# Optimization experiments

Hardware: AMD Instinct MI355X
Metric: run time of the kernel (lower is better)

## Reference

```python
import jax, jax.numpy as jnp
import numpy as np

B, NSP, H, W = 8, 1024, 256, 256   # frames, superpixels/frame, label-map size
N = B * NSP                        # total superpixel nodes
MIX = 0.5                          # mixing_coeff
SIGMA = 0.05


def _interp_axis(x, out, axis):
    # 1-D bilinear interpolation along `axis`, align_corners=True
    n = x.shape[axis]
    pos = jnp.linspace(0.0, n - 1.0, out).astype(x.dtype)
    i0 = jnp.floor(pos).astype(jnp.int32)
    i1 = jnp.minimum(i0 + 1, n - 1)
    wt = pos - i0.astype(x.dtype)
    shp = [1] * x.ndim
    shp[axis] = out
    wt = wt.reshape(shp)
    return jnp.take(x, i0, axis=axis) * (1 - wt) + jnp.take(x, i1, axis=axis) * wt


def _upsample_ac(x, oh, ow):
    # nn.UpsamplingBilinear2d (align_corners=True)
    if x.shape[2] == oh and x.shape[3] == ow:
        return x
    return _interp_axis(_interp_axis(x, oh, 2), ow, 3)


def _sp_pool(feats, seg):
    # upsample [B,C,h,w] to label resolution, then average features per superpixel -> [N, C]
    C = feats.shape[1]
    up = _upsample_ac(feats, H, W)
    vals = up.transpose(0, 2, 3, 1).reshape(-1, C)          # [B*H*W, C]
    sums = jax.ops.segment_sum(vals, seg, num_segments=N)
    cnt = jax.ops.segment_sum(jnp.ones((seg.shape[0],), vals.dtype), seg, num_segments=N)
    return sums / jnp.maximum(cnt, 1.0)[:, None]


def _gcn(x, Wm, b, src, dst, ew):
    # GCNConv(normalize=False): out_i = sum_{j->i} ew * (x_j @ W) + b
    h = x @ Wm
    agg = jax.ops.segment_sum(h[src] * ew[:, None], dst, num_segments=x.shape[0])
    return agg + b


def _coord_map():
    # channel 0 varies along dim2 (w), channel 1 varies along dim3 (h), both in [0,1]
    c0 = jnp.broadcast_to((jnp.arange(H, dtype=jnp.float32) / (H - 1))[:, None], (H, W))
    c1 = jnp.broadcast_to((jnp.arange(W, dtype=jnp.float32) / (W - 1))[None, :], (H, W))
    return jnp.broadcast_to(jnp.stack([c0, c1], 0)[None], (B, 2, H, W))


def setup_inputs() -> dict:
    key = jax.random.key(0)
    ks = jax.random.split(key, 12)
    labels = jax.random.randint(ks[0], (B, 1, H, W), 0, NSP, dtype=jnp.int32)
    skip0 = jax.random.normal(ks[1], (B, 512, 32, 32), jnp.float32)
    skip1 = jax.random.normal(ks[2], (B, 256, 64, 64), jnp.float32)
    skip2 = jax.random.normal(ks[3], (B, 256, 128, 128), jnp.float32)
    E = 131072
    edges_nn = jax.random.randint(ks[4], (2, E), 0, N, dtype=jnp.int32)
    negs = jax.random.randint(ks[5], (E,), 0, N, dtype=jnp.int32)
    W0 = jax.random.normal(ks[6], (512, 256), jnp.float32) / np.float32(np.sqrt(512))
    W1 = jax.random.normal(ks[7], (256, 256), jnp.float32) / np.float32(np.sqrt(256))
    W2 = jax.random.normal(ks[8], (256, 256), jnp.float32) / np.float32(np.sqrt(256))
    lin_w = jax.random.normal(ks[9], (256, 1), jnp.float32) / np.float32(np.sqrt(256))
    z = jnp.zeros((256,), jnp.float32)
    return {"labels": labels, "skip0": skip0, "skip1": skip1, "skip2": skip2,
            "edges_nn": edges_nn, "negs": negs,
            "W0": W0, "b0": z, "W1": W1, "b1": z, "W2": W2, "b2": z, "lin_w": lin_w}


def reference(labels, skip0, skip1, skip2, edges_nn, negs, W0, b0, W1, b1, W2, b2, lin_w):
    # per-pixel global superpixel id (offset per frame)
    seg = (labels.reshape(B, -1) + NSP * jnp.arange(B, dtype=labels.dtype)[:, None]).reshape(-1)
    src, dst = edges_nn[0], edges_nn[1]

    # pooled normalized coordinates per superpixel -> gaussian edge weights
    pc = _sp_pool(_coord_map(), seg)                        # [N, 2]
    dr = pc[src] - pc[dst]
    dist = jnp.linalg.norm(dr, axis=1)
    edge_attr = jnp.exp(-dist ** 2 / SIGMA)

    x = _sp_pool(skip0, seg)                                # [N, 512]
    layers = [(W0, b0, None), (W1, b1, skip1), (W2, b2, skip2)]
    for i, (Wm, b, sk) in enumerate(layers):
        if i > 0:
            x = (1 - MIX) * x + MIX * _sp_pool(sk, seg)
        x = jax.nn.relu(_gcn(x, Wm, b, src, dst, edge_attr))

    s = x @ lin_w                                           # [N, 1]
    dap = jax.nn.sigmoid(s[src] - s[dst])
    dan = jax.nn.sigmoid(s[src] - s[negs])
    return dan, dap, edge_attr
```

## Files before the change

### kernel.cpp

```cpp
#include <hip/hip_runtime.h>
#include <hip/hip_fp16.h>
#include <cstdint>
#include <cstddef>

#define BB 8
#define NSPX 1024
#define NNODE 8192
#define EE 131072
#define NPIX 524288
#define CH 256

typedef unsigned int uint;
typedef unsigned long long u64;

__device__ __forceinline__ uint packh2(float a, float b) {
  __half2 h = __float22half2_rn(make_float2(a, b));
  return *reinterpret_cast<uint*>(&h);
}
__device__ __forceinline__ __half2 uh2(uint u) { return *reinterpret_cast<__half2*>(&u); }
__device__ __forceinline__ uint h2u(__half2 h) { return *reinterpret_cast<uint*>(&h); }

__global__ __launch_bounds__(256) void zero_kernel(int4* p, int n4) {
  int i = blockIdx.x * 256 + threadIdx.x;
  int stride = gridDim.x * 256;
  int4 z = make_int4(0, 0, 0, 0);
  for (; i < n4; i += stride) p[i] = z;
}

__device__ __forceinline__ void dev_transpose_h(const float* __restrict__ src, __half* __restrict__ dst,
                                                int C, int P, int b, int p0, int c0, int t,
                                                uint (*tile)[33]) {
  int l16 = t & 15, r16 = t >> 4;
#pragma unroll
  for (int pass = 0; pass < 4; ++pass) {
    int c = r16 + pass * 16;
    float4 v = *(const float4*)&src[((size_t)b * C + c0 + c) * P + p0 + l16 * 4];
    tile[c][l16 * 2]     = packh2(v.x, v.y);
    tile[c][l16 * 2 + 1] = packh2(v.z, v.w);
  }
  __syncthreads();
  int l8 = t & 7, r32 = t >> 3;
#pragma unroll
  for (int pass = 0; pass < 2; ++pass) {
    int p = r32 + pass * 32;
    int ph = p >> 1;
    int odd = p & 1;
    uint r[4];
#pragma unroll
    for (int q = 0; q < 4; ++q) {
      uint ua = tile[l8 * 8 + 2 * q][ph];
      uint ub = tile[l8 * 8 + 2 * q + 1][ph];
      r[q] = odd ? ((ua >> 16) | (ub & 0xFFFF0000u))
                 : ((ua & 0xFFFFu) | (ub << 16));
    }
    *(uint4*)&dst[((size_t)b * P + p0 + p) * C + c0 + l8 * 8] = make_uint4(r[0], r[1], r[2], r[3]);
  }
}

__global__ __launch_bounds__(256) void t2_kernel(const float* __restrict__ src, __half* __restrict__ dst) {
  __shared__ uint tile[64][33];
  int idx = blockIdx.x;
  int p0 = (idx & 255) * 64;
  int c0 = ((idx >> 8) & 3) * 64;
  int b = idx >> 10;
  dev_transpose_h(src, dst, 256, 16384, b, p0, c0, threadIdx.x, tile);
}

__device__ __forceinline__ void dev_gemm_kmaj(const float* __restrict__ A, const float* __restrict__ W,
                                              __half* __restrict__ out, int idx, int t,
                                              float (*As)[36]) {
  int b = idx >> 6;
  int m0 = (idx & 31) * 32;
  int n0 = ((idx >> 5) & 1) * 128;
  int ct = t & 31;
  int rm = t >> 5;
  int l8 = t & 7, kr = t >> 3;
  const float* Ab = A + (size_t)b * 512 * 1024;
  float4 acc[4];
#pragma unroll
  for (int i = 0; i < 4; ++i) acc[i] = make_float4(0.f, 0.f, 0.f, 0.f);
  for (int k0 = 0; k0 < 512; k0 += 64) {
#pragma unroll
    for (int pass = 0; pass < 2; ++pass) {
      int k = kr + pass * 32;
      float4 v = *(const float4*)&Ab[(size_t)(k0 + k) * 1024 + m0 + l8 * 4];
      *(float4*)&As[k][l8 * 4] = v;
    }
    __syncthreads();
#pragma unroll 8
    for (int k = 0; k < 64; ++k) {
      float4 a = *(const float4*)&As[k][rm * 4];
      float4 wv = *(const float4*)&W[(size_t)(k0 + k) * 256 + n0 + ct * 4];
      acc[0].x += a.x * wv.x; acc[0].y += a.x * wv.y; acc[0].z += a.x * wv.z; acc[0].w += a.x * wv.w;
      acc[1].x += a.y * wv.x; acc[1].y += a.y * wv.y; acc[1].z += a.y * wv.z; acc[1].w += a.y * wv.w;
      acc[2].x += a.z * wv.x; acc[2].y += a.z * wv.y; acc[2].z += a.z * wv.z; acc[2].w += a.z * wv.w;
      acc[3].x += a.w * wv.x; acc[3].y += a.w * wv.y; acc[3].z += a.w * wv.z; acc[3].w += a.w * wv.w;
    }
    __syncthreads();
  }
#pragma unroll
  for (int i = 0; i < 4; ++i) {
    int m = m0 + rm * 4 + i;
    uint2 pk = make_uint2(packh2(acc[i].x, acc[i].y), packh2(acc[i].z, acc[i].w));
    *(uint2*)&out[((size_t)b * 1024 + m) * 256 + n0 + ct * 4] = pk;
  }
}

__global__ __launch_bounds__(256) void fusedA2_kernel(const int* __restrict__ labels,
                                                      const int* __restrict__ edst,
                                                      int* __restrict__ segb,
                                                      u64* __restrict__ packed,
                                                      int* __restrict__ cnt_e,
                                                      const float* __restrict__ skip0,
                                                      const float* __restrict__ W0,
                                                      __half* __restrict__ F0b,
                                                      const float* __restrict__ skip1,
                                                      __half* __restrict__ F1t) {
  __shared__ __align__(16) char smem[9216];
  int blk = blockIdx.x;
  int t = threadIdx.x;
  int s = blk % 10;
  int q = blk / 10;
  if (s < 4) {
    int idx = q * 4 + s;
    int p0 = (idx & 63) * 64;
    int c0 = ((idx >> 6) & 3) * 64;
    int b = idx >> 8;
    dev_transpose_h(skip1, F1t, 256, 4096, b, p0, c0, t, (uint(*)[33])smem);
  } else if (s < 9) {
    int idx = q * 5 + (s - 4);
    if (idx < 2048) {
      int p = idx * 256 + t;
      int b = p >> 16;
      int h = (p >> 8) & 255;
      int w = p & 255;
      int seg = labels[p] + (b << 10);
      segb[p] = seg;
      u64 enc = (1ULL << 48) | ((u64)h << 24) | (u64)w;
      atomicAdd(&packed[seg], enc);
    } else {
      int e = (idx - 2048) * 256 + t;
      atomicAdd(&cnt_e[edst[e]], 1);
    }
  } else {
    dev_gemm_kmaj(skip0, W0, F0b, q, t, (float(*)[36])smem);
  }
}

__global__ __launch_bounds__(1024) void fusedB_kernel(const u64* __restrict__ packed,
                                                      const int* __restrict__ cnt_e,
                                                      int* __restrict__ poff, int* __restrict__ eoff,
                                                      float* __restrict__ rcnt,
                                                      float* __restrict__ pch, float* __restrict__ pcw) {
  int blk = blockIdx.x;
  int t = threadIdx.x;
  if (blk < 2) {
    __shared__ int ps[1024];
    int which = blk;
    int* coff = which ? eoff : poff;
    int base = t * 8;
    int v[8];
    int sum = 0;
#pragma unroll
    for (int i = 0; i < 8; ++i) {
      int x = which ? cnt_e[base + i] : (int)(packed[base + i] >> 48);
      v[i] = sum;
      sum += x;
    }
    ps[t] = sum;
    __syncthreads();
    for (int off = 1; off < 1024; off <<= 1) {
      int x = (t >= off) ? ps[t - off] : 0;
      __syncthreads();
      ps[t] += x;
      __syncthreads();
    }
    int prev = (t == 0) ? 0 : ps[t - 1];
#pragma unroll
    for (int i = 0; i < 8; ++i) coff[base + i] = prev + v[i];
    if (t == 1023) coff[8192] = ps[1023];
  } else {
    int n = (blk - 2) * 1024 + t;
    u64 v = packed[n];
    int c = (int)(v >> 48);
    int sh = (int)((v >> 24) & 0xFFFFFF);
    int sw = (int)(v & 0xFFFFFF);
    float r = 1.0f / (float)(c > 1 ? c : 1);
    rcnt[n] = r;
    pch[n] = (float)sh * r * (1.0f / 255.0f);
    pcw[n] = (float)sw * r * (1.0f / 255.0f);
  }
}

__global__ __launch_bounds__(256) void scatter2_kernel(const int* __restrict__ segb,
                                                       const int* __restrict__ poff,
                                                       int* __restrict__ pcur,
                                                       int* __restrict__ psorted,
                                                       const int* __restrict__ esrc,
                                                       const int* __restrict__ edst,
                                                       const float* __restrict__ pch,
                                                       const float* __restrict__ pcw,
                                                       const int* __restrict__ eoff,
                                                       int* __restrict__ ecur,
                                                       uint2* __restrict__ evw,
                                                       float* __restrict__ outp) {
  int blk = blockIdx.x;
  int t = threadIdx.x;
  if (blk < 2048) {
    int p = blk * 256 + t;
    int s = segb[p];
    int pos = poff[s] + atomicAdd(&pcur[s], 1);
    psorted[pos] = p;
  } else {
    int e = (blk - 2048) * 256 + t;
    int s1 = esrc[e], d1 = edst[e];
    float dh = pch[s1] - pch[d1];
    float dw = pcw[s1] - pcw[d1];
    float ea = expf(-(dh * dh + dw * dw) * 20.0f);
    outp[2 * EE + e] = ea;
    int pos = eoff[d1] + atomicAdd(&ecur[d1], 1);
    evw[pos] = make_uint2((uint)s1, __float_as_uint(ea));
  }
}

__device__ __forceinline__ void tap16(const __half* __restrict__ tp, float wt, __half2* acc) {
  uint4 qa = *(const uint4*)tp;
  uint4 qb = *(const uint4*)(tp + 8);
  __half2 W = __float2half2_rn(wt);
  acc[0] = __hfma2(W, uh2(qa.x), acc[0]);
  acc[1] = __hfma2(W, uh2(qa.y), acc[1]);
  acc[2] = __hfma2(W, uh2(qa.z), acc[2]);
  acc[3] = __hfma2(W, uh2(qa.w), acc[3]);
  acc[4] = __hfma2(W, uh2(qb.x), acc[4]);
  acc[5] = __hfma2(W, uh2(qb.y), acc[5]);
  acc[6] = __hfma2(W, uh2(qb.z), acc[6]);
  acc[7] = __hfma2(W, uh2(qb.w), acc[7]);
}

template <int HS>
__device__ __forceinline__ void taps16(const __half* __restrict__ fb, int h, int w, __half2* acc) {
  const float fh = (float)(HS - 1) / 255.0f;
  float ph = h * fh, pw = w * fh;
  int i0 = (int)ph, j0 = (int)pw;
  float th = ph - (float)i0, tw = pw - (float)j0;
  int i1 = min(i0 + 1, HS - 1), jj1 = min(j0 + 1, HS - 1);
  float w11 = th * tw, w10 = th - w11, w01 = tw - w11, w00 = 1.f - th - tw + w11;
  tap16(fb + (i0 * HS + j0) * 256, w00, acc);
  tap16(fb + (i0 * HS + jj1) * 256, w01, acc);
  tap16(fb + (i1 * HS + j0) * 256, w10, acc);
  tap16(fb + (i1 * HS + jj1) * 256, w11, acc);
}

__global__ __launch_bounds__(256) void fusedC_kernel(const __half* __restrict__ F0,
                                                     const __half* __restrict__ F1,
                                                     const __half* __restrict__ F2,
                                                     const int* __restrict__ poff,
                                                     const int* __restrict__ psorted,
                                                     const float* __restrict__ rc,
                                                     __half* __restrict__ p0out,
                                                     float* __restrict__ p1out,
                                                     float* __restrict__ p2out) {
  __shared__ __align__(16) char smem[18432];
  int blk = blockIdx.x;
  int t = threadIdx.x;
  if (blk >= 8192 && blk < 16384) {
    int x = blk - 8192;
    int n = ((x & 7) << 10) | (x >> 3);
    int b = n >> 10;
    int l = t & 15;
    int s = t >> 4;
    const __half* f0 = F0 + (size_t)b * 1024 * 256 + l * 16;
    const __half* f1 = F1 + (size_t)b * 4096 * 256 + l * 16;
    int j1 = poff[n + 1];
    __half2 z = __float2half2_rn(0.f);
    __half2 a0[8], a1[8];
#pragma unroll
    for (int i = 0; i < 8; ++i) { a0[i] = z; a1[i] = z; }
    for (int j = poff[n] + s; j < j1; j += 16) {
      int p = psorted[j];
      int h = (p >> 8) & 255, w = p & 255;
      taps16<32>(f0, h, w, a0);
      taps16<64>(f1, h, w, a1);
    }
    uint (*red)[256][9] = (uint(*)[256][9])smem;
#pragma unroll
    for (int k = 0; k < 8; ++k) { red[0][t][k] = h2u(a0[k]); red[1][t][k] = h2u(a1[k]); }
    __syncthreads();
    if (t < 128) {
      int l2 = t >> 3, k = t & 7;
      float r = rc[n];
      float2 s0 = make_float2(0.f, 0.f), s1 = s0;
#pragma unroll
      for (int ss = 0; ss < 16; ++ss) {
        float2 v0 = __half22float2(uh2(red[0][ss * 16 + l2][k]));
        float2 v1 = __half22float2(uh2(red[1][ss * 16 + l2][k]));
        s0.x += v0.x; s0.y += v0.y;
        s1.x += v1.x; s1.y += v1.y;
      }
      int c = l2 * 16 + k * 2;
      *(uint*)&p0out[(size_t)n * 256 + c] = packh2(s0.x * r, s0.y * r);
      *(float2*)&p1out[(size_t)n * 256 + c] = make_float2(s1.x * r, s1.y * r);
    }
  } else {
    int x, c0;
    if (blk < 8192) { x = blk; c0 = 0; }
    else            { x = blk - 16384; c0 = 128; }
    int n = ((x & 7) << 10) | (x >> 3);
    int b = n >> 10;
    int l = t & 7;
    int s = t >> 3;
    const __half* fb = F2 + (size_t)b * 16384 * 256 + c0 + l * 16;
    int j1 = poff[n + 1];
    __half2 z = __float2half2_rn(0.f);
    __half2 acc[8];
#pragma unroll
    for (int i = 0; i < 8; ++i) acc[i] = z;
    for (int j = poff[n] + s; j < j1; j += 32) {
      int p = psorted[j];
      int h = (p >> 8) & 255, w = p & 255;
      taps16<128>(fb, h, w, acc);
    }
    uint (*red)[9] = (uint(*)[9])smem;
#pragma unroll
    for (int k = 0; k < 8; ++k) red[t][k] = h2u(acc[k]);
    __syncthreads();
    if (t < 64) {
      int l2 = t >> 3, k = t & 7;
      float r = rc[n];
      float2 sm = make_float2(0.f, 0.f);
#pragma unroll
      for (int ss = 0; ss < 32; ++ss) {
        float2 v = __half22float2(uh2(red[ss * 8 + l2][k]));
        sm.x += v.x; sm.y += v.y;
      }
      int c = c0 + l2 * 16 + k * 2;
      *(float2*)&p2out[(size_t)n * 256 + c] = make_float2(sm.x * r, sm.y * r);
    }
  }
}

__global__ __launch_bounds__(256) void gemm_mix_n256(const float* __restrict__ X, const float* __restrict__ Pl,
                                                     const float* __restrict__ W, __half* __restrict__ out) {
  const int t = threadIdx.x;
  const int r0 = blockIdx.x * 16;
  const int cw = (t & 63) * 4;
  const int rg = (t >> 6) * 4;
  __shared__ float Xl[16][68];
  float4 acc[4];
#pragma unroll
  for (int i = 0; i < 4; ++i) acc[i] = make_float4(0.f, 0.f, 0.f, 0.f);
  for (int k0 = 0; k0 < 256; k0 += 64) {
#pragma unroll
    for (int l = 0; l < 4; ++l) {
      int idx = t + 256 * l;
      int r = idx >> 6, k = idx & 63;
      size_t a = (size_t)(r0 + r) * 256 + k0 + k;
      Xl[r][k] = 0.5f * (X[a] + Pl[a]);
    }
    __syncthreads();
#pragma unroll
    for (int k4 = 0; k4 < 64; k4 += 4) {
      float4 a[4];
#pragma unroll
      for (int i = 0; i < 4; ++i) a[i] = *(const float4*)&Xl[rg + i][k4];
#pragma unroll
      for (int kk = 0; kk < 4; ++kk) {
        float4 w = *(const float4*)&W[(size_t)(k0 + k4 + kk) * 256 + cw];
#pragma unroll
        for (int i = 0; i < 4; ++i) {
          float av = ((const float*)&a[i])[kk];
          acc[i].x += av * w.x;
          acc[i].y += av * w.y;
          acc[i].z += av * w.z;
          acc[i].w += av * w.w;
        }
      }
    }
    __syncthreads();
  }
#pragma unroll
  for (int i = 0; i < 4; ++i) {
    uint2 pk = make_uint2(packh2(acc[i].x, acc[i].y), packh2(acc[i].z, acc[i].w));
    *(uint2*)&out[(size_t)(r0 + rg + i) * 256 + cw] = pk;
  }
}

__global__ __launch_bounds__(256) void agg_kernel(const __half* __restrict__ h, const float* __restrict__ bias,
                                                  const int* __restrict__ eoff,
                                                  const uint2* __restrict__ evw,
                                                  float* __restrict__ xout) {
  int n = blockIdx.x * 2 + (threadIdx.x >> 7);
  int c2 = threadIdx.x & 127;
  int e0 = eoff[n], e1 = eoff[n + 1];
  float a0 = 0.f, a1 = 0.f;
  for (int j = e0; j < e1; ++j) {
    uint2 ev = evw[j];
    float wv = __uint_as_float(ev.y);
    uint hv = *(const uint*)&h[((size_t)ev.x << 8) + c2 * 2];
    float2 f = __half22float2(uh2(hv));
    a0 += wv * f.x;
    a1 += wv * f.y;
  }
  float v0 = a0 + bias[2 * c2];
  float v1 = a1 + bias[2 * c2 + 1];
  float2 st = make_float2(v0 > 0.f ? v0 : 0.f, v1 > 0.f ? v1 : 0.f);
  *(float2*)&xout[((size_t)n << 8) + 2 * c2] = st;
}

__global__ __launch_bounds__(256) void score_kernel(const float* __restrict__ x, const float* __restrict__ lw,
                                                    float* __restrict__ s) {
  int t = threadIdx.x;
  int n = blockIdx.x * 4 + (t >> 6);
  int lane = t & 63;
  const float* row = x + ((size_t)n << 8);
  float v = row[lane] * lw[lane] + row[lane + 64] * lw[lane + 64] +
            row[lane + 128] * lw[lane + 128] + row[lane + 192] * lw[lane + 192];
#pragma unroll
  for (int off = 32; off > 0; off >>= 1) v += __shfl_down(v, off, 64);
  if (lane == 0) s[n] = v;
}

__global__ __launch_bounds__(256) void out_kernel(const float* __restrict__ s, const int* __restrict__ src,
                                                  const int* __restrict__ dst, const int* __restrict__ negs,
                                                  float* __restrict__ outp) {
  int e = blockIdx.x * 256 + threadIdx.x;
  if (e >= EE) return;
  float ss = s[src[e]];
  float a = ss - s[negs[e]];
  float b = ss - s[dst[e]];
  outp[e] = 1.0f / (1.0f + expf(-a));
  outp[EE + e] = 1.0f / (1.0f + expf(-b));
}

extern "C" void kernel_launch(void* const* d_in, const int* in_sizes, int n_in,
                              void* d_out, int out_size, void* d_ws, size_t ws_size,
                              hipStream_t stream) {
  const int*   labels = (const int*)d_in[0];
  const float* skip0  = (const float*)d_in[1];
  const float* skip1  = (const float*)d_in[2];
  const float* skip2  = (const float*)d_in[3];
  const int*   edges  = (const int*)d_in[4];
  const int*   negs   = (const int*)d_in[5];
  const float* W0     = (const float*)d_in[6];
  const float* b0     = (const float*)d_in[7];
  const float* W1     = (const float*)d_in[8];
  const float* b1     = (const float*)d_in[9];
  const float* W2     = (const float*)d_in[10];
  const float* b2     = (const float*)d_in[11];
  const float* lw     = (const float*)d_in[12];
  const int* esrc = edges;
  const int* edst = edges + EE;
  float* outp = (float*)d_out;

  size_t o = 0;
  char* base = (char*)d_ws;
  auto alloc = [&](size_t bytes) -> void* {
    void* p = base + o;
    o += (bytes + 255) & ~(size_t)255;
    return p;
  };
  u64* packed  = (u64*)alloc(NNODE * 8);
  int* cnt_e   = (int*)alloc(NNODE * 4);
  int* ecur    = (int*)alloc(NNODE * 4);
  int* pcur    = (int*)alloc(NNODE * 4);
  size_t zbytes = o;
  float*  rcnt    = (float*)alloc(NNODE * 4);
  float*  pch     = (float*)alloc(NNODE * 4);
  float*  pcw     = (float*)alloc(NNODE * 4);
  int*    poff    = (int*)alloc((NNODE + 1) * 4);
  int*    eoff    = (int*)alloc((NNODE + 1) * 4);
  uint2*  evw     = (uint2*)alloc((size_t)EE * 8);
  int*    psorted = (int*)alloc(NPIX * 4);
  int*    segb    = (int*)alloc(NPIX * 4);
  float*  bufA    = (float*)alloc((size_t)NNODE * CH * 4);
  float*  bufB    = (float*)alloc((size_t)NNODE * CH * 4);
  float*  p1buf   = (float*)alloc((size_t)NNODE * CH * 4);
  float*  p2buf   = (float*)alloc((size_t)NNODE * CH * 4);
  __half* h0b     = (__half*)alloc((size_t)NNODE * CH * 2);
  __half* h1b     = (__half*)alloc((size_t)NNODE * CH * 2);
  __half* F0b     = (__half*)alloc((size_t)BB * 1024 * CH * 2);
  __half* F1t     = (__half*)alloc((size_t)BB * 4096 * CH * 2);
  __half* F2t     = (__half*)alloc((size_t)BB * 16384 * CH * 2);
  float*  sbuf    = (float*)alloc(NNODE * 4);
  (void)ws_size; (void)n_in; (void)in_sizes; (void)out_size;

  zero_kernel<<<64, 256, 0, stream>>>((int4*)d_ws, (int)(zbytes / 16));
  fusedA2_kernel<<<5120, 256, 0, stream>>>(labels, edst, segb, packed, cnt_e,
                                           skip0, W0, F0b, skip1, F1t);
  t2_kernel<<<8192, 256, 0, stream>>>(skip2, F2t);
  fusedB_kernel<<<10, 1024, 0, stream>>>(packed, cnt_e, poff, eoff, rcnt, pch, pcw);
  scatter2_kernel<<<2048 + 512, 256, 0, stream>>>(segb, poff, pcur, psorted,
                                                  esrc, edst, pch, pcw, eoff, ecur, evw, outp);
  fusedC_kernel<<<24576, 256, 0, stream>>>(F0b, F1t, F2t, poff, psorted, rcnt,
                                           h0b, p1buf, p2buf);
  agg_kernel<<<NNODE / 2, 256, 0, stream>>>(h0b, b0, eoff, evw, bufB);
  gemm_mix_n256<<<NNODE / 16, 256, 0, stream>>>(bufB, p1buf, W1, h1b);
  agg_kernel<<<NNODE / 2, 256, 0, stream>>>(h1b, b1, eoff, evw, bufA);
  gemm_mix_n256<<<NNODE / 16, 256, 0, stream>>>(bufA, p2buf, W2, h1b);
  agg_kernel<<<NNODE / 2, 256, 0, stream>>>(h1b, b2, eoff, evw, bufB);
  score_kernel<<<NNODE / 4, 256, 0, stream>>>(bufB, lw, sbuf);
  out_kernel<<<EE / 256, 256, 0, stream>>>(sbuf, esrc, edst, negs, outp);
}
```

Before: 731.0 us.

## Fuse GCN tail into one cooperative kernel and regroup transpose launches

The seven small tail launches (three aggregations, two mix GEMMs, score, output) become a single cooperative persistent kernel of 1024 blocks that uses grid-wide syncs between stages. If the cooperative launch fails, it falls back to the original separate launches. The skip2 and skip1 transposes move out of the first fused kernel and the standalone transpose kernel into the pixel-scatter and edge-weight kernel. The aim is to cut launch gaps and overlap the memory-bound transposes with the atomic scatter work, at the cost of grid-sync overhead and fewer active blocks per stage.

```diff
diff --git a/kernel.cpp b/kernel.cpp
--- a/kernel.cpp
+++ b/kernel.cpp
@@ -1,7 +1,10 @@
 #include <hip/hip_runtime.h>
 #include <hip/hip_fp16.h>
+#include <hip/hip_cooperative_groups.h>
 #include <cstdint>
 #include <cstddef>
+
+namespace cg = cooperative_groups;
 
 #define BB 8
 #define NSPX 1024
@@ -55,15 +58,6 @@
     }
     *(uint4*)&dst[((size_t)b * P + p0 + p) * C + c0 + l8 * 8] = make_uint4(r[0], r[1], r[2], r[3]);
   }
-}
-
-__global__ __launch_bounds__(256) void t2_kernel(const float* __restrict__ src, __half* __restrict__ dst) {
-  __shared__ uint tile[64][33];
-  int idx = blockIdx.x;
-  int p0 = (idx & 255) * 64;
-  int c0 = ((idx >> 8) & 3) * 64;
-  int b = idx >> 10;
-  dev_transpose_h(src, dst, 256, 16384, b, p0, c0, threadIdx.x, tile);
 }
 
 __device__ __forceinline__ void dev_gemm_kmaj(const float* __restrict__ A, const float* __restrict__ W,
@@ -106,31 +100,20 @@
   }
 }
 
-__global__ __launch_bounds__(256) void fusedA2_kernel(const int* __restrict__ labels,
+__global__ __launch_bounds__(256) void fusedA3_kernel(const int* __restrict__ labels,
                                                       const int* __restrict__ edst,
                                                       int* __restrict__ segb,
                                                       u64* __restrict__ packed,
                                                       int* __restrict__ cnt_e,
                                                       const float* __restrict__ skip0,
                                                       const float* __restrict__ W0,
-                                                      __half* __restrict__ F0b,
-                                                      const float* __restrict__ skip1,
-                                                      __half* __restrict__ F1t) {
-  __shared__ __align__(16) char smem[9216];
+                                                      __half* __restrict__ F0b) {
+  __shared__ __align__(16) float As[64][36];
   int blk = blockIdx.x;
   int t = threadIdx.x;
-  int s = blk % 10;
-  int q = blk / 10;
-  if (s < 4) {
-    int idx = q * 4 + s;
-    int p0 = (idx & 63) * 64;
-    int c0 = ((idx >> 6) & 3) * 64;
-    int b = idx >> 8;
-    dev_transpose_h(skip1, F1t, 256, 4096, b, p0, c0, t, (uint(*)[33])smem);
-  } else if (s < 9) {
-    int idx = q * 5 + (s - 4);
-    if (idx < 2048) {
-      int p = idx * 256 + t;
+  if (blk < 2560) {
+    if (blk < 2048) {
+      int p = blk * 256 + t;
       int b = p >> 16;
       int h = (p >> 8) & 255;
       int w = p & 255;
@@ -139,11 +122,11 @@
       u64 enc = (1ULL << 48) | ((u64)h << 24) | (u64)w;
       atomicAdd(&packed[seg], enc);
     } else {
-      int e = (idx - 2048) * 256 + t;
+      int e = (blk - 2048) * 256 + t;
       atomicAdd(&cnt_e[edst[e]], 1);
     }
   } else {
-    dev_gemm_kmaj(skip0, W0, F0b, q, t, (float(*)[36])smem);
+    dev_gemm_kmaj(skip0, W0, F0b, blk - 2560, t, As);
   }
 }
 
@@ -192,34 +175,57 @@
   }
 }
 
-__global__ __launch_bounds__(256) void scatter2_kernel(const int* __restrict__ segb,
-                                                       const int* __restrict__ poff,
-                                                       int* __restrict__ pcur,
-                                                       int* __restrict__ psorted,
-                                                       const int* __restrict__ esrc,
-                                                       const int* __restrict__ edst,
-                                                       const float* __restrict__ pch,
-                                                       const float* __restrict__ pcw,
-                                                       const int* __restrict__ eoff,
-                                                       int* __restrict__ ecur,
-                                                       uint2* __restrict__ evw,
-                                                       float* __restrict__ outp) {
+__global__ __launch_bounds__(256) void fusedT_kernel(const float* __restrict__ skip1,
+                                                     __half* __restrict__ F1t,
+                                                     const float* __restrict__ skip2,
+                                                     __half* __restrict__ F2t,
+                                                     const int* __restrict__ segb,
+                                                     const int* __restrict__ poff,
+                                                     int* __restrict__ pcur,
+                                                     int* __restrict__ psorted,
+                                                     const int* __restrict__ esrc,
+                                                     const int* __restrict__ edst,
+                                                     const float* __restrict__ pch,
+                                                     const float* __restrict__ pcw,
+                                                     const int* __restrict__ eoff,
+                                                     int* __restrict__ ecur,
+                                                     uint2* __restrict__ evw,
+                                                     float* __restrict__ outp) {
+  __shared__ uint tile[64][33];
   int blk = blockIdx.x;
   int t = threadIdx.x;
-  if (blk < 2048) {
-    int p = blk * 256 + t;
-    int s = segb[p];
-    int pos = poff[s] + atomicAdd(&pcur[s], 1);
-    psorted[pos] = p;
+  int s = blk % 5;
+  int q = blk / 5;
+  if (s < 4) {
+    int idx = q * 4 + s;
+    if (idx < 8192) {
+      int p0 = (idx & 255) * 64;
+      int c0 = ((idx >> 8) & 3) * 64;
+      int b = idx >> 10;
+      dev_transpose_h(skip2, F2t, 256, 16384, b, p0, c0, t, tile);
+    } else {
+      int i2 = idx - 8192;
+      int p0 = (i2 & 63) * 64;
+      int c0 = ((i2 >> 6) & 3) * 64;
+      int b = i2 >> 8;
+      dev_transpose_h(skip1, F1t, 256, 4096, b, p0, c0, t, tile);
+    }
   } else {
-    int e = (blk - 2048) * 256 + t;
-    int s1 = esrc[e], d1 = edst[e];
-    float dh = pch[s1] - pch[d1];
-    float dw = pcw[s1] - pcw[d1];
-    float ea = expf(-(dh * dh + dw * dw) * 20.0f);
-    outp[2 * EE + e] = ea;
-    int pos = eoff[d1] + atomicAdd(&ecur[d1], 1);
-    evw[pos] = make_uint2((uint)s1, __float_as_uint(ea));
+    if (q < 2048) {
+      int p = q * 256 + t;
+      int sg = segb[p];
+      int pos = poff[sg] + atomicAdd(&pcur[sg], 1);
+      psorted[pos] = p;
+    } else {
+      int e = (q - 2048) * 256 + t;
+      int s1 = esrc[e], d1 = edst[e];
+      float dh = pch[s1] - pch[d1];
+      float dw = pcw[s1] - pcw[d1];
+      float ea = expf(-(dh * dh + dw * dw) * 20.0f);
+      outp[2 * EE + e] = ea;
+      int pos = eoff[d1] + atomicAdd(&ecur[d1], 1);
+      evw[pos] = make_uint2((uint)s1, __float_as_uint(ea));
+    }
   }
 }
 
@@ -339,58 +345,11 @@
   }
 }
 
-__global__ __launch_bounds__(256) void gemm_mix_n256(const float* __restrict__ X, const float* __restrict__ Pl,
-                                                     const float* __restrict__ W, __half* __restrict__ out) {
-  const int t = threadIdx.x;
-  const int r0 = blockIdx.x * 16;
-  const int cw = (t & 63) * 4;
-  const int rg = (t >> 6) * 4;
-  __shared__ float Xl[16][68];
-  float4 acc[4];
-#pragma unroll
-  for (int i = 0; i < 4; ++i) acc[i] = make_float4(0.f, 0.f, 0.f, 0.f);
-  for (int k0 = 0; k0 < 256; k0 += 64) {
-#pragma unroll
-    for (int l = 0; l < 4; ++l) {
-      int idx = t + 256 * l;
-      int r = idx >> 6, k = idx & 63;
-      size_t a = (size_t)(r0 + r) * 256 + k0 + k;
-      Xl[r][k] = 0.5f * (X[a] + Pl[a]);
-    }
-    __syncthreads();
-#pragma unroll
-    for (int k4 = 0; k4 < 64; k4 += 4) {
-      float4 a[4];
-#pragma unroll
-      for (int i = 0; i < 4; ++i) a[i] = *(const float4*)&Xl[rg + i][k4];
-#pragma unroll
-      for (int kk = 0; kk < 4; ++kk) {
-        float4 w = *(const float4*)&W[(size_t)(k0 + k4 + kk) * 256 + cw];
-#pragma unroll
-        for (int i = 0; i < 4; ++i) {
-          float av = ((const float*)&a[i])[kk];
-          acc[i].x += av * w.x;
-          acc[i].y += av * w.y;
-          acc[i].z += av * w.z;
-          acc[i].w += av * w.w;
-        }
-      }
-    }
-    __syncthreads();
-  }
-#pragma unroll
-  for (int i = 0; i < 4; ++i) {
-    uint2 pk = make_uint2(packh2(acc[i].x, acc[i].y), packh2(acc[i].z, acc[i].w));
-    *(uint2*)&out[(size_t)(r0 + rg + i) * 256 + cw] = pk;
-  }
-}
-
-__global__ __launch_bounds__(256) void agg_kernel(const __half* __restrict__ h, const float* __restrict__ bias,
-                                                  const int* __restrict__ eoff,
-                                                  const uint2* __restrict__ evw,
-                                                  float* __restrict__ xout) {
-  int n = blockIdx.x * 2 + (threadIdx.x >> 7);
-  int c2 = threadIdx.x & 127;
+__device__ __forceinline__ void agg_body(const __half* h, const float* bias,
+                                         const int* eoff, const uint2* evw,
+                                         float* xout, int pr, int t) {
+  int n = pr * 2 + (t >> 7);
+  int c2 = t & 127;
   int e0 = eoff[n], e1 = eoff[n + 1];
   float a0 = 0.f, a1 = 0.f;
   for (int j = e0; j < e1; ++j) {
@@ -403,14 +362,56 @@
   }
   float v0 = a0 + bias[2 * c2];
   float v1 = a1 + bias[2 * c2 + 1];
-  float2 st = make_float2(v0 > 0.f ? v0 : 0.f, v1 > 0.f ? v1 : 0.f);
-  *(float2*)&xout[((size_t)n << 8) + 2 * c2] = st;
-}
-
-__global__ __launch_bounds__(256) void score_kernel(const float* __restrict__ x, const float* __restrict__ lw,
-                                                    float* __restrict__ s) {
-  int t = threadIdx.x;
-  int n = blockIdx.x * 4 + (t >> 6);
+  *(float2*)&xout[((size_t)n << 8) + 2 * c2] =
+      make_float2(v0 > 0.f ? v0 : 0.f, v1 > 0.f ? v1 : 0.f);
+}
+
+__device__ __forceinline__ void gemm_body(const float* X, const float* Pl, const float* W,
+                                          __half* out, int tilei, int t, float (*Xl)[68]) {
+  const int r0 = tilei * 16;
+  const int cw = (t & 63) * 4;
+  const int rg = (t >> 6) * 4;
+  float4 acc[4];
+#pragma unroll
+  for (int i = 0; i < 4; ++i) acc[i] = make_float4(0.f, 0.f, 0.f, 0.f);
+  for (int k0 = 0; k0 < 256; k0 += 64) {
+#pragma unroll
+    for (int l = 0; l < 4; ++l) {
+      int idx = t + 256 * l;
+      int r = idx >> 6, k = idx & 63;
+      size_t a = (size_t)(r0 + r) * 256 + k0 + k;
+      Xl[r][k] = 0.5f * (X[a] + Pl[a]);
+    }
+    __syncthreads();
+#pragma unroll
+    for (int k4 = 0; k4 < 64; k4 += 4) {
+      float4 a[4];
+#pragma unroll
+      for (int i = 0; i < 4; ++i) a[i] = *(const float4*)&Xl[rg + i][k4];
+#pragma unroll
+      for (int kk = 0; kk < 4; ++kk) {
+        float4 w = *(const float4*)&W[(size_t)(k0 + k4 + kk) * 256 + cw];
+#pragma unroll
+        for (int i = 0; i < 4; ++i) {
+          float av = ((const float*)&a[i])[kk];
+          acc[i].x += av * w.x;
+          acc[i].y += av * w.y;
+          acc[i].z += av * w.z;
+          acc[i].w += av * w.w;
+        }
+      }
+    }
+    __syncthreads();
+  }
+#pragma unroll
+  for (int i = 0; i < 4; ++i) {
+    uint2 pk = make_uint2(packh2(acc[i].x, acc[i].y), packh2(acc[i].z, acc[i].w));
+    *(uint2*)&out[(size_t)(r0 + rg + i) * 256 + cw] = pk;
+  }
+}
+
+__device__ __forceinline__ void score_body(const float* x, const float* lw, float* s, int g, int t) {
+  int n = g * 4 + (t >> 6);
   int lane = t & 63;
   const float* row = x + ((size_t)n << 8);
   float v = row[lane] * lw[lane] + row[lane + 64] * lw[lane + 64] +
@@ -418,6 +419,60 @@
 #pragma unroll
   for (int off = 32; off > 0; off >>= 1) v += __shfl_down(v, off, 64);
   if (lane == 0) s[n] = v;
+}
+
+__global__ __launch_bounds__(256, 4) void coop_tail(const __half* h0, const float* b0,
+                                                    const float* b1, const float* b2,
+                                                    const float* W1, const float* W2,
+                                                    const float* lw,
+                                                    const int* eoff, const uint2* evw,
+                                                    const float* p1, const float* p2,
+                                                    float* xA, float* xB, __half* hbuf,
+                                                    float* sbuf,
+                                                    const int* esrc, const int* edst,
+                                                    const int* negs, float* outp) {
+  cg::grid_group grid = cg::this_grid();
+  __shared__ float Xl[16][68];
+  int bid = blockIdx.x;
+  int t = threadIdx.x;
+  for (int pr = bid; pr < 4096; pr += 1024) agg_body(h0, b0, eoff, evw, xB, pr, t);
+  grid.sync();
+  if (bid < 512) gemm_body(xB, p1, W1, hbuf, bid, t, Xl);
+  grid.sync();
+  for (int pr = bid; pr < 4096; pr += 1024) agg_body(hbuf, b1, eoff, evw, xA, pr, t);
+  grid.sync();
+  if (bid < 512) gemm_body(xA, p2, W2, hbuf, bid, t, Xl);
+  grid.sync();
+  for (int pr = bid; pr < 4096; pr += 1024) agg_body(hbuf, b2, eoff, evw, xB, pr, t);
+  grid.sync();
+  for (int g = bid; g < 2048; g += 1024) score_body(xB, lw, sbuf, g, t);
+  grid.sync();
+  for (int g = bid; g < 512; g += 1024) {
+    int e = g * 256 + t;
+    float ss = sbuf[esrc[e]];
+    float a = ss - sbuf[negs[e]];
+    float b = ss - sbuf[edst[e]];
+    outp[e] = 1.0f / (1.0f + expf(-a));
+    outp[EE + e] = 1.0f / (1.0f + expf(-b));
+  }
+}
+
+__global__ __launch_bounds__(256) void agg_kernel(const __half* __restrict__ h, const float* __restrict__ bias,
+                                                  const int* __restrict__ eoff,
+                                                  const uint2* __restrict__ evw,
+                                                  float* __restrict__ xout) {
+  agg_body(h, bias, eoff, evw, xout, blockIdx.x, threadIdx.x);
+}
+
+__global__ __launch_bounds__(256) void gemm_mix_n256(const float* __restrict__ X, const float* __restrict__ Pl,
+                                                     const float* __restrict__ W, __half* __restrict__ out) {
+  __shared__ float Xl[16][68];
+  gemm_body(X, Pl, W, out, blockIdx.x, threadIdx.x, Xl);
+}
+
+__global__ __launch_bounds__(256) void score_kernel(const float* __restrict__ x, const float* __restrict__ lw,
+                                                    float* __restrict__ s) {
+  score_body(x, lw, s, blockIdx.x, threadIdx.x);
 }
 
 __global__ __launch_bounds__(256) void out_kernel(const float* __restrict__ s, const int* __restrict__ src,
@@ -485,19 +540,29 @@
   (void)ws_size; (void)n_in; (void)in_sizes; (void)out_size;
 
   zero_kernel<<<64, 256, 0, stream>>>((int4*)d_ws, (int)(zbytes / 16));
-  fusedA2_kernel<<<5120, 256, 0, stream>>>(labels, edst, segb, packed, cnt_e,
-                                           skip0, W0, F0b, skip1, F1t);
-  t2_kernel<<<8192, 256, 0, stream>>>(skip2, F2t);
+  fusedA3_kernel<<<3072, 256, 0, stream>>>(labels, edst, segb, packed, cnt_e,
+                                           skip0, W0, F0b);
   fusedB_kernel<<<10, 1024, 0, stream>>>(packed, cnt_e, poff, eoff, rcnt, pch, pcw);
-  scatter2_kernel<<<2048 + 512, 256, 0, stream>>>(segb, poff, pcur, psorted,
-                                                  esrc, edst, pch, pcw, eoff, ecur, evw, outp);
+  fusedT_kernel<<<12800, 256, 0, stream>>>(skip1, F1t, skip2, F2t,
+                                           segb, poff, pcur, psorted,
+                                           esrc, edst, pch, pcw, eoff, ecur, evw, outp);
   fusedC_kernel<<<24576, 256, 0, stream>>>(F0b, F1t, F2t, poff, psorted, rcnt,
                                            h0b, p1buf, p2buf);
-  agg_kernel<<<NNODE / 2, 256, 0, stream>>>(h0b, b0, eoff, evw, bufB);
-  gemm_mix_n256<<<NNODE / 16, 256, 0, stream>>>(bufB, p1buf, W1, h1b);
-  agg_kernel<<<NNODE / 2, 256, 0, stream>>>(h1b, b1, eoff, evw, bufA);
-  gemm_mix_n256<<<NNODE / 16, 256, 0, stream>>>(bufA, p2buf, W2, h1b);
-  agg_kernel<<<NNODE / 2, 256, 0, stream>>>(h1b, b2, eoff, evw, bufB);
-  score_kernel<<<NNODE / 4, 256, 0, stream>>>(bufB, lw, sbuf);
-  out_kernel<<<EE / 256, 256, 0, stream>>>(sbuf, esrc, edst, negs, outp);
-}
+  void* cargs[] = {(void*)&h0b, (void*)&b0, (void*)&b1, (void*)&b2,
+                   (void*)&W1, (void*)&W2, (void*)&lw,
+                   (void*)&eoff, (void*)&evw, (void*)&p1buf, (void*)&p2buf,
+                   (void*)&bufA, (void*)&bufB, (void*)&h1b, (void*)&sbuf,
+                   (void*)&esrc, (void*)&edst, (void*)&negs, (void*)&outp};
+  hipError_t cerr = hipLaunchCooperativeKernel((const void*)coop_tail,
+                                               dim3(1024), dim3(256), cargs, 0, stream);
+  if (cerr != hipSuccess) {
+    (void)hipGetLastError();
+    agg_kernel<<<NNODE / 2, 256, 0, stream>>>(h0b, b0, eoff, evw, bufB);
+    gemm_mix_n256<<<NNODE / 16, 256, 0, stream>>>(bufB, p1buf, W1, h1b);
+    agg_kernel<<<NNODE / 2, 256, 0, stream>>>(h1b, b1, eoff, evw, bufA);
+    gemm_mix_n256<<<NNODE / 16, 256, 0, stream>>>(bufA, p2buf, W2, h1b);
+    agg_kernel<<<NNODE / 2, 256, 0, stream>>>(h1b, b2, eoff, evw, bufB);
+    score_kernel<<<NNODE / 4, 256, 0, stream>>>(bufB, lw, sbuf);
+    out_kernel<<<EE / 256, 256, 0, stream>>>(sbuf, esrc, edst, negs, outp);
+  }
+}
```

After: 1.423 ms. +94.6%, slower.

## Regroup launch schedule: fuse transposes and gemm with scatter, fuse final agg with score

Applied to the files above, without the earlier changes.

Splits the counting atomics into their own small kernel and moves the skip1/skip2 transposes and the skip0 gemm into one combined kernel with the pixel/edge scatter, running after the prefix-sum stage. It also fuses the last aggregation with the score dot product so the final node features never go to memory. The aim is fewer launches and better overlap of bandwidth-heavy transposes with the atomic-bound scatter. The trade-off is that the large transposes now wait until the counting and prefix stages finish instead of running alongside them.

```diff
diff --git a/kernel.cpp b/kernel.cpp
--- a/kernel.cpp
+++ b/kernel.cpp
@@ -27,123 +27,25 @@
   for (; i < n4; i += stride) p[i] = z;
 }
 
-__device__ __forceinline__ void dev_transpose_h(const float* __restrict__ src, __half* __restrict__ dst,
-                                                int C, int P, int b, int p0, int c0, int t,
-                                                uint (*tile)[33]) {
-  int l16 = t & 15, r16 = t >> 4;
-#pragma unroll
-  for (int pass = 0; pass < 4; ++pass) {
-    int c = r16 + pass * 16;
-    float4 v = *(const float4*)&src[((size_t)b * C + c0 + c) * P + p0 + l16 * 4];
-    tile[c][l16 * 2]     = packh2(v.x, v.y);
-    tile[c][l16 * 2 + 1] = packh2(v.z, v.w);
-  }
-  __syncthreads();
-  int l8 = t & 7, r32 = t >> 3;
-#pragma unroll
-  for (int pass = 0; pass < 2; ++pass) {
-    int p = r32 + pass * 32;
-    int ph = p >> 1;
-    int odd = p & 1;
-    uint r[4];
-#pragma unroll
-    for (int q = 0; q < 4; ++q) {
-      uint ua = tile[l8 * 8 + 2 * q][ph];
-      uint ub = tile[l8 * 8 + 2 * q + 1][ph];
-      r[q] = odd ? ((ua >> 16) | (ub & 0xFFFF0000u))
-                 : ((ua & 0xFFFFu) | (ub << 16));
-    }
-    *(uint4*)&dst[((size_t)b * P + p0 + p) * C + c0 + l8 * 8] = make_uint4(r[0], r[1], r[2], r[3]);
-  }
-}
-
-__global__ __launch_bounds__(256) void t2_kernel(const float* __restrict__ src, __half* __restrict__ dst) {
-  __shared__ uint tile[64][33];
-  int idx = blockIdx.x;
-  int p0 = (idx & 255) * 64;
-  int c0 = ((idx >> 8) & 3) * 64;
-  int b = idx >> 10;
-  dev_transpose_h(src, dst, 256, 16384, b, p0, c0, threadIdx.x, tile);
-}
-
-__device__ __forceinline__ void dev_gemm_kmaj(const float* __restrict__ A, const float* __restrict__ W,
-                                              __half* __restrict__ out, int idx, int t,
-                                              float (*As)[36]) {
-  int b = idx >> 6;
-  int m0 = (idx & 31) * 32;
-  int n0 = ((idx >> 5) & 1) * 128;
-  int ct = t & 31;
-  int rm = t >> 5;
-  int l8 = t & 7, kr = t >> 3;
-  const float* Ab = A + (size_t)b * 512 * 1024;
-  float4 acc[4];
-#pragma unroll
-  for (int i = 0; i < 4; ++i) acc[i] = make_float4(0.f, 0.f, 0.f, 0.f);
-  for (int k0 = 0; k0 < 512; k0 += 64) {
-#pragma unroll
-    for (int pass = 0; pass < 2; ++pass) {
-      int k = kr + pass * 32;
-      float4 v = *(const float4*)&Ab[(size_t)(k0 + k) * 1024 + m0 + l8 * 4];
-      *(float4*)&As[k][l8 * 4] = v;
-    }
-    __syncthreads();
-#pragma unroll 8
-    for (int k = 0; k < 64; ++k) {
-      float4 a = *(const float4*)&As[k][rm * 4];
-      float4 wv = *(const float4*)&W[(size_t)(k0 + k) * 256 + n0 + ct * 4];
-      acc[0].x += a.x * wv.x; acc[0].y += a.x * wv.y; acc[0].z += a.x * wv.z; acc[0].w += a.x * wv.w;
-      acc[1].x += a.y * wv.x; acc[1].y += a.y * wv.y; acc[1].z += a.y * wv.z; acc[1].w += a.y * wv.w;
-      acc[2].x += a.z * wv.x; acc[2].y += a.z * wv.y; acc[2].z += a.z * wv.z; acc[2].w += a.z * wv.w;
-      acc[3].x += a.w * wv.x; acc[3].y += a.w * wv.y; acc[3].z += a.w * wv.z; acc[3].w += a.w * wv.w;
-    }
-    __syncthreads();
-  }
-#pragma unroll
-  for (int i = 0; i < 4; ++i) {
-    int m = m0 + rm * 4 + i;
-    uint2 pk = make_uint2(packh2(acc[i].x, acc[i].y), packh2(acc[i].z, acc[i].w));
-    *(uint2*)&out[((size_t)b * 1024 + m) * 256 + n0 + ct * 4] = pk;
-  }
-}
-
-__global__ __launch_bounds__(256) void fusedA2_kernel(const int* __restrict__ labels,
-                                                      const int* __restrict__ edst,
-                                                      int* __restrict__ segb,
-                                                      u64* __restrict__ packed,
-                                                      int* __restrict__ cnt_e,
-                                                      const float* __restrict__ skip0,
-                                                      const float* __restrict__ W0,
-                                                      __half* __restrict__ F0b,
-                                                      const float* __restrict__ skip1,
-                                                      __half* __restrict__ F1t) {
-  __shared__ __align__(16) char smem[9216];
+__global__ __launch_bounds__(256) void cnt2_kernel(const int* __restrict__ labels,
+                                                   const int* __restrict__ edst,
+                                                   int* __restrict__ segb,
+                                                   u64* __restrict__ packed,
+                                                   int* __restrict__ cnt_e) {
   int blk = blockIdx.x;
   int t = threadIdx.x;
-  int s = blk % 10;
-  int q = blk / 10;
-  if (s < 4) {
-    int idx = q * 4 + s;
-    int p0 = (idx & 63) * 64;
-    int c0 = ((idx >> 6) & 3) * 64;
-    int b = idx >> 8;
-    dev_transpose_h(skip1, F1t, 256, 4096, b, p0, c0, t, (uint(*)[33])smem);
-  } else if (s < 9) {
-    int idx = q * 5 + (s - 4);
-    if (idx < 2048) {
-      int p = idx * 256 + t;
-      int b = p >> 16;
-      int h = (p >> 8) & 255;
-      int w = p & 255;
-      int seg = labels[p] + (b << 10);
-      segb[p] = seg;
-      u64 enc = (1ULL << 48) | ((u64)h << 24) | (u64)w;
-      atomicAdd(&packed[seg], enc);
-    } else {
-      int e = (idx - 2048) * 256 + t;
-      atomicAdd(&cnt_e[edst[e]], 1);
-    }
+  if (blk < 2048) {
+    int p = blk * 256 + t;
+    int b = p >> 16;
+    int h = (p >> 8) & 255;
+    int w = p & 255;
+    int seg = labels[p] + (b << 10);
+    segb[p] = seg;
+    u64 enc = (1ULL << 48) | ((u64)h << 24) | (u64)w;
+    atomicAdd(&packed[seg], enc);
   } else {
-    dev_gemm_kmaj(skip0, W0, F0b, q, t, (float(*)[36])smem);
+    int e = (blk - 2048) * 256 + t;
+    atomicAdd(&cnt_e[edst[e]], 1);
   }
 }
 
@@ -192,34 +94,134 @@
   }
 }
 
-__global__ __launch_bounds__(256) void scatter2_kernel(const int* __restrict__ segb,
-                                                       const int* __restrict__ poff,
-                                                       int* __restrict__ pcur,
-                                                       int* __restrict__ psorted,
-                                                       const int* __restrict__ esrc,
-                                                       const int* __restrict__ edst,
-                                                       const float* __restrict__ pch,
-                                                       const float* __restrict__ pcw,
-                                                       const int* __restrict__ eoff,
-                                                       int* __restrict__ ecur,
-                                                       uint2* __restrict__ evw,
-                                                       float* __restrict__ outp) {
+__device__ __forceinline__ void dev_transpose_h(const float* __restrict__ src, __half* __restrict__ dst,
+                                                int C, int P, int b, int p0, int c0, int t,
+                                                uint (*tile)[33]) {
+  int l16 = t & 15, r16 = t >> 4;
+#pragma unroll
+  for (int pass = 0; pass < 4; ++pass) {
+    int c = r16 + pass * 16;
+    float4 v = *(const float4*)&src[((size_t)b * C + c0 + c) * P + p0 + l16 * 4];
+    tile[c][l16 * 2]     = packh2(v.x, v.y);
+    tile[c][l16 * 2 + 1] = packh2(v.z, v.w);
+  }
+  __syncthreads();
+  int l8 = t & 7, r32 = t >> 3;
+#pragma unroll
+  for (int pass = 0; pass < 2; ++pass) {
+    int p = r32 + pass * 32;
+    int ph = p >> 1;
+    int odd = p & 1;
+    uint r[4];
+#pragma unroll
+    for (int q = 0; q < 4; ++q) {
+      uint ua = tile[l8 * 8 + 2 * q][ph];
+      uint ub = tile[l8 * 8 + 2 * q + 1][ph];
+      r[q] = odd ? ((ua >> 16) | (ub & 0xFFFF0000u))
+                 : ((ua & 0xFFFFu) | (ub << 16));
+    }
+    *(uint4*)&dst[((size_t)b * P + p0 + p) * C + c0 + l8 * 8] = make_uint4(r[0], r[1], r[2], r[3]);
+  }
+}
+
+__device__ __forceinline__ void dev_gemm_kmaj(const float* __restrict__ A, const float* __restrict__ W,
+                                              __half* __restrict__ out, int idx, int t,
+                                              float (*As)[36]) {
+  int b = idx >> 6;
+  int m0 = (idx & 31) * 32;
+  int n0 = ((idx >> 5) & 1) * 128;
+  int ct = t & 31;
+  int rm = t >> 5;
+  int l8 = t & 7, kr = t >> 3;
+  const float* Ab = A + (size_t)b * 512 * 1024;
+  float4 acc[4];
+#pragma unroll
+  for (int i = 0; i < 4; ++i) acc[i] = make_float4(0.f, 0.f, 0.f, 0.f);
+  for (int k0 = 0; k0 < 512; k0 += 64) {
+#pragma unroll
+    for (int pass = 0; pass < 2; ++pass) {
+      int k = kr + pass * 32;
+      float4 v = *(const float4*)&Ab[(size_t)(k0 + k) * 1024 + m0 + l8 * 4];
+      *(float4*)&As[k][l8 * 4] = v;
+    }
+    __syncthreads();
+#pragma unroll 8
+    for (int k = 0; k < 64; ++k) {
+      float4 a = *(const float4*)&As[k][rm * 4];
+      float4 wv = *(const float4*)&W[(size_t)(k0 + k) * 256 + n0 + ct * 4];
+      acc[0].x += a.x * wv.x; acc[0].y += a.x * wv.y; acc[0].z += a.x * wv.z; acc[0].w += a.x * wv.w;
+      acc[1].x += a.y * wv.x; acc[1].y += a.y * wv.y; acc[1].z += a.y * wv.z; acc[1].w += a.y * wv.w;
+      acc[2].x += a.z * wv.x; acc[2].y += a.z * wv.y; acc[2].z += a.z * wv.z; acc[2].w += a.z * wv.w;
+      acc[3].x += a.w * wv.x; acc[3].y += a.w * wv.y; acc[3].z += a.w * wv.z; acc[3].w += a.w * wv.w;
+    }
+    __syncthreads();
+  }
+#pragma unroll
+  for (int i = 0; i < 4; ++i) {
+    int m = m0 + rm * 4 + i;
+    uint2 pk = make_uint2(packh2(acc[i].x, acc[i].y), packh2(acc[i].z, acc[i].w));
+    *(uint2*)&out[((size_t)b * 1024 + m) * 256 + n0 + ct * 4] = pk;
+  }
+}
+
+__global__ __launch_bounds__(256) void fusedT_kernel(const float* __restrict__ skip1,
+                                                     __half* __restrict__ F1t,
+                                                     const float* __restrict__ skip2,
+                                                     __half* __restrict__ F2t,
+                                                     const float* __restrict__ skip0,
+                                                     const float* __restrict__ W0,
+                                                     __half* __restrict__ F0b,
+                                                     const int* __restrict__ segb,
+                                                     const int* __restrict__ poff,
+                                                     int* __restrict__ pcur,
+                                                     int* __restrict__ psorted,
+                                                     const int* __restrict__ esrc,
+                                                     const int* __restrict__ edst,
+                                                     const float* __restrict__ pch,
+                                                     const float* __restrict__ pcw,
+                                                     const int* __restrict__ eoff,
+                                                     int* __restrict__ ecur,
+                                                     uint2* __restrict__ evw,
+                                                     float* __restrict__ outp) {
+  __shared__ __align__(16) char smem[9216];
   int blk = blockIdx.x;
   int t = threadIdx.x;
-  if (blk < 2048) {
-    int p = blk * 256 + t;
-    int s = segb[p];
-    int pos = poff[s] + atomicAdd(&pcur[s], 1);
-    psorted[pos] = p;
+  if (blk >= 12800) {
+    dev_gemm_kmaj(skip0, W0, F0b, blk - 12800, t, (float(*)[36])smem);
+    return;
+  }
+  int s = blk % 5;
+  int q = blk / 5;
+  if (s < 4) {
+    int idx = q * 4 + s;
+    if (idx < 8192) {
+      int p0 = (idx & 255) * 64;
+      int c0 = ((idx >> 8) & 3) * 64;
+      int b = idx >> 10;
+      dev_transpose_h(skip2, F2t, 256, 16384, b, p0, c0, t, (uint(*)[33])smem);
+    } else {
+      int i2 = idx - 8192;
+      int p0 = (i2 & 63) * 64;
+      int c0 = ((i2 >> 6) & 3) * 64;
+      int b = i2 >> 8;
+      dev_transpose_h(skip1, F1t, 256, 4096, b, p0, c0, t, (uint(*)[33])smem);
+    }
   } else {
-    int e = (blk - 2048) * 256 + t;
-    int s1 = esrc[e], d1 = edst[e];
-    float dh = pch[s1] - pch[d1];
-    float dw = pcw[s1] - pcw[d1];
-    float ea = expf(-(dh * dh + dw * dw) * 20.0f);
-    outp[2 * EE + e] = ea;
-    int pos = eoff[d1] + atomicAdd(&ecur[d1], 1);
-    evw[pos] = make_uint2((uint)s1, __float_as_uint(ea));
+    if (q < 2048) {
+      int p = q * 256 + t;
+      int sg = segb[p];
+      int pos = poff[sg] + atomicAdd(&pcur[sg], 1);
+      psorted[pos] = p;
+    } else {
+      int e = (q - 2048) * 256 + t;
+      int s1 = esrc[e], d1 = edst[e];
+      float dh = pch[s1] - pch[d1];
+      float dw = pcw[s1] - pcw[d1];
+      float ea = expf(-(dh * dh + dw * dw) * 20.0f);
+      outp[2 * EE + e] = ea;
+      int pos = eoff[d1] + atomicAdd(&ecur[d1], 1);
+      evw[pos] = make_uint2((uint)s1, __float_as_uint(ea));
+    }
   }
 }
 
@@ -339,52 +341,6 @@
   }
 }
 
-__global__ __launch_bounds__(256) void gemm_mix_n256(const float* __restrict__ X, const float* __restrict__ Pl,
-                                                     const float* __restrict__ W, __half* __restrict__ out) {
-  const int t = threadIdx.x;
-  const int r0 = blockIdx.x * 16;
-  const int cw = (t & 63) * 4;
-  const int rg = (t >> 6) * 4;
-  __shared__ float Xl[16][68];
-  float4 acc[4];
-#pragma unroll
-  for (int i = 0; i < 4; ++i) acc[i] = make_float4(0.f, 0.f, 0.f, 0.f);
-  for (int k0 = 0; k0 < 256; k0 += 64) {
-#pragma unroll
-    for (int l = 0; l < 4; ++l) {
-      int idx = t + 256 * l;
-      int r = idx >> 6, k = idx & 63;
-      size_t a = (size_t)(r0 + r) * 256 + k0 + k;
-      Xl[r][k] = 0.5f * (X[a] + Pl[a]);
-    }
-    __syncthreads();
-#pragma unroll
-    for (int k4 = 0; k4 < 64; k4 += 4) {
-      float4 a[4];
-#pragma unroll
-      for (int i = 0; i < 4; ++i) a[i] = *(const float4*)&Xl[rg + i][k4];
-#pragma unroll
-      for (int kk = 0; kk < 4; ++kk) {
-        float4 w = *(const float4*)&W[(size_t)(k0 + k4 + kk) * 256 + cw];
-#pragma unroll
-        for (int i = 0; i < 4; ++i) {
-          float av = ((const float*)&a[i])[kk];
-          acc[i].x += av * w.x;
-          acc[i].y += av * w.y;
-          acc[i].z += av * w.z;
-          acc[i].w += av * w.w;
-        }
-      }
-    }
-    __syncthreads();
-  }
-#pragma unroll
-  for (int i = 0; i < 4; ++i) {
-    uint2 pk = make_uint2(packh2(acc[i].x, acc[i].y), packh2(acc[i].z, acc[i].w));
-    *(uint2*)&out[(size_t)(r0 + rg + i) * 256 + cw] = pk;
-  }
-}
-
 __global__ __launch_bounds__(256) void agg_kernel(const __half* __restrict__ h, const float* __restrict__ bias,
                                                   const int* __restrict__ eoff,
                                                   const uint2* __restrict__ evw,
@@ -403,21 +359,87 @@
   }
   float v0 = a0 + bias[2 * c2];
   float v1 = a1 + bias[2 * c2 + 1];
-  float2 st = make_float2(v0 > 0.f ? v0 : 0.f, v1 > 0.f ? v1 : 0.f);
-  *(float2*)&xout[((size_t)n << 8) + 2 * c2] = st;
-}
-
-__global__ __launch_bounds__(256) void score_kernel(const float* __restrict__ x, const float* __restrict__ lw,
-                                                    float* __restrict__ s) {
+  *(float2*)&xout[((size_t)n << 8) + 2 * c2] =
+      make_float2(v0 > 0.f ? v0 : 0.f, v1 > 0.f ? v1 : 0.f);
+}
+
+__global__ __launch_bounds__(256) void agg_score_kernel(const __half* __restrict__ h,
+                                                        const float* __restrict__ bias,
+                                                        const int* __restrict__ eoff,
+                                                        const uint2* __restrict__ evw,
+                                                        const float* __restrict__ lw,
+                                                        float* __restrict__ s) {
   int t = threadIdx.x;
-  int n = blockIdx.x * 4 + (t >> 6);
-  int lane = t & 63;
-  const float* row = x + ((size_t)n << 8);
-  float v = row[lane] * lw[lane] + row[lane + 64] * lw[lane + 64] +
-            row[lane + 128] * lw[lane + 128] + row[lane + 192] * lw[lane + 192];
-#pragma unroll
-  for (int off = 32; off > 0; off >>= 1) v += __shfl_down(v, off, 64);
-  if (lane == 0) s[n] = v;
+  int n = blockIdx.x * 2 + (t >> 7);
+  int c2 = t & 127;
+  int e0 = eoff[n], e1 = eoff[n + 1];
+  float a0 = 0.f, a1 = 0.f;
+  for (int j = e0; j < e1; ++j) {
+    uint2 ev = evw[j];
+    float wv = __uint_as_float(ev.y);
+    uint hv = *(const uint*)&h[((size_t)ev.x << 8) + c2 * 2];
+    float2 f = __half22float2(uh2(hv));
+    a0 += wv * f.x;
+    a1 += wv * f.y;
+  }
+  float v0 = a0 + bias[2 * c2];
+  float v1 = a1 + bias[2 * c2 + 1];
+  v0 = v0 > 0.f ? v0 : 0.f;
+  v1 = v1 > 0.f ? v1 : 0.f;
+  float p = v0 * lw[2 * c2] + v1 * lw[2 * c2 + 1];
+#pragma unroll
+  for (int off = 32; off > 0; off >>= 1) p += __shfl_down(p, off, 64);
+  __shared__ float ws[4];
+  if ((t & 63) == 0) ws[t >> 6] = p;
+  __syncthreads();
+  if (t == 0)   s[n] = ws[0] + ws[1];
+  if (t == 128) s[n] = ws[2] + ws[3];
+}
+
+__global__ __launch_bounds__(256) void gemm_mix_n256(const float* __restrict__ X, const float* __restrict__ Pl,
+                                                     const float* __restrict__ W, __half* __restrict__ out) {
+  const int t = threadIdx.x;
+  const int r0 = blockIdx.x * 16;
+  const int cw = (t & 63) * 4;
+  const int rg = (t >> 6) * 4;
+  __shared__ float Xl[16][68];
+  float4 acc[4];
+#pragma unroll
+  for (int i = 0; i < 4; ++i) acc[i] = make_float4(0.f, 0.f, 0.f, 0.f);
+  for (int k0 = 0; k0 < 256; k0 += 64) {
+#pragma unroll
+    for (int l = 0; l < 4; ++l) {
+      int idx = t + 256 * l;
+      int r = idx >> 6, k = idx & 63;
+      size_t a = (size_t)(r0 + r) * 256 + k0 + k;
+      Xl[r][k] = 0.5f * (X[a] + Pl[a]);
+    }
+    __syncthreads();
+#pragma unroll
+    for (int k4 = 0; k4 < 64; k4 += 4) {
+      float4 a[4];
+#pragma unroll
+      for (int i = 0; i < 4; ++i) a[i] = *(const float4*)&Xl[rg + i][k4];
+#pragma unroll
+      for (int kk = 0; kk < 4; ++kk) {
+        float4 w = *(const float4*)&W[(size_t)(k0 + k4 + kk) * 256 + cw];
+#pragma unroll
+        for (int i = 0; i < 4; ++i) {
+          float av = ((const float*)&a[i])[kk];
+          acc[i].x += av * w.x;
+          acc[i].y += av * w.y;
+          acc[i].z += av * w.z;
+          acc[i].w += av * w.w;
+        }
+      }
+    }
+    __syncthreads();
+  }
+#pragma unroll
+  for (int i = 0; i < 4; ++i) {
+    uint2 pk = make_uint2(packh2(acc[i].x, acc[i].y), packh2(acc[i].z, acc[i].w));
+    *(uint2*)&out[(size_t)(r0 + rg + i) * 256 + cw] = pk;
+  }
 }
 
 __global__ __launch_bounds__(256) void out_kernel(const float* __restrict__ s, const int* __restrict__ src,
@@ -485,19 +507,17 @@
   (void)ws_size; (void)n_in; (void)in_sizes; (void)out_size;
 
   zero_kernel<<<64, 256, 0, stream>>>((int4*)d_ws, (int)(zbytes / 16));
-  fusedA2_kernel<<<5120, 256, 0, stream>>>(labels, edst, segb, packed, cnt_e,
-                                           skip0, W0, F0b, skip1, F1t);
-  t2_kernel<<<8192, 256, 0, stream>>>(skip2, F2t);
+  cnt2_kernel<<<2048 + 512, 256, 0, stream>>>(labels, edst, segb, packed, cnt_e);
   fusedB_kernel<<<10, 1024, 0, stream>>>(packed, cnt_e, poff, eoff, rcnt, pch, pcw);
-  scatter2_kernel<<<2048 + 512, 256, 0, stream>>>(segb, poff, pcur, psorted,
-                                                  esrc, edst, pch, pcw, eoff, ecur, evw, outp);
+  fusedT_kernel<<<13312, 256, 0, stream>>>(skip1, F1t, skip2, F2t, skip0, W0, F0b,
+                                           segb, poff, pcur, psorted,
+                                           esrc, edst, pch, pcw, eoff, ecur, evw, outp);
   fusedC_kernel<<<24576, 256, 0, stream>>>(F0b, F1t, F2t, poff, psorted, rcnt,
                                            h0b, p1buf, p2buf);
   agg_kernel<<<NNODE / 2, 256, 0, stream>>>(h0b, b0, eoff, evw, bufB);
   gemm_mix_n256<<<NNODE / 16, 256, 0, stream>>>(bufB, p1buf, W1, h1b);
   agg_kernel<<<NNODE / 2, 256, 0, stream>>>(h1b, b1, eoff, evw, bufA);
   gemm_mix_n256<<<NNODE / 16, 256, 0, stream>>>(bufA, p2buf, W2, h1b);
-  agg_kernel<<<NNODE / 2, 256, 0, stream>>>(h1b, b2, eoff, evw, bufB);
-  score_kernel<<<NNODE / 4, 256, 0, stream>>>(bufB, lw, sbuf);
+  agg_score_kernel<<<NNODE / 2, 256, 0, stream>>>(h1b, b2, eoff, evw, lw, sbuf);
   out_kernel<<<EE / 256, 256, 0, stream>>>(sbuf, esrc, edst, negs, outp);
 }
```

New measurement: 691.5 us. -5.4%, faster.
